# Kernel optimization log

Measured on AMD Instinct MI355X. Metric: run time of the kernel, lower is better.

The kernel has to match this reference:

```python
import jax, jax.numpy as jnp
import numpy as np
from jax import lax

B, L, V = 128, 64, 8192
E = H = 128
STEPS = 10
MAX_BIN = 512
BETA_START, BETA_END = 1e-4, 2e-2


def setup_inputs():
    key = jax.random.key(0)
    k = jax.random.split(key, 23)
    s = 0.05
    padded_x = (jax.random.uniform(k[0], (B, L, V)) < 0.01).astype(jnp.float32)
    lengths = jax.random.randint(k[1], (B,), 1, L + 1)
    visit_mask = (jnp.arange(L)[None, :] < lengths[:, None]).astype(jnp.float32)
    padded_bins = jnp.sort(jax.random.randint(k[2], (B, L), 0, MAX_BIN), axis=1)
    t_diff = jax.random.randint(k[3], (B,), 1, STEPS + 1)
    eps = jax.random.normal(k[4], (B, L, E))
    z0 = jax.random.normal(k[5], (B, L, E))
    noise = jax.random.normal(k[6], (STEPS, B, L, E))
    W_visit = jax.random.normal(k[7], (E, V)) * s
    bin_embed = (jax.random.normal(k[8], (MAX_BIN + 2, E)) * s).at[0].set(0.0)  # padding_idx=0
    W_ih = jax.random.normal(k[9], (4 * H, E)) * s
    W_hh = jax.random.normal(k[10], (4 * H, H)) * s
    b_ih = jax.random.normal(k[11], (4 * H,)) * s
    b_hh = jax.random.normal(k[12], (4 * H,)) * s
    W_cls = jax.random.normal(k[13], (1, H)) * s
    b_cls = jax.random.normal(k[14], (1,)) * s
    W_proj = jax.random.normal(k[15], (E, H)) * s
    time_embed = jax.random.normal(k[16], (STEPS + 1, E)) * s
    W_fuse = jax.random.normal(k[17], (2, 2 * E)) * s
    b_fuse = jax.random.normal(k[18], (2,)) * s
    W_e1 = jax.random.normal(k[19], (E, 2 * E)) * s
    b_e1 = jax.random.normal(k[20], (E,)) * s
    W_e2 = jax.random.normal(k[21], (E, E)) * s
    b_e2 = jax.random.normal(k[22], (E,)) * s
    return dict(padded_x=padded_x, visit_mask=visit_mask, padded_bins=padded_bins,
                t_diff=t_diff, eps=eps, z0=z0, noise=noise, W_visit=W_visit,
                bin_embed=bin_embed, W_ih=W_ih, W_hh=W_hh, b_ih=b_ih, b_hh=b_hh,
                W_cls=W_cls, b_cls=b_cls, W_proj=W_proj, time_embed=time_embed,
                W_fuse=W_fuse, b_fuse=b_fuse, W_e1=W_e1, b_e1=b_e1, W_e2=W_e2, b_e2=b_e2)


def _lstm(v, W_ih, W_hh, b_ih, b_hh):
    # v: [B,L,E] -> h: [B,L,H]; PyTorch gate order i,f,g,o
    xg = jnp.einsum('ble,ge->blg', v, W_ih) + b_ih + b_hh
    def step(carry, x):
        h, c = carry
        g = x + h @ W_hh.T
        i, f, gg, o = jnp.split(g, 4, axis=-1)
        c = jax.nn.sigmoid(f) * c + jax.nn.sigmoid(i) * jnp.tanh(gg)
        h = jax.nn.sigmoid(o) * jnp.tanh(c)
        return (h, c), h
    z = jnp.zeros((v.shape[0], W_hh.shape[1]), v.dtype)
    _, hs = lax.scan(step, (z, z), jnp.swapaxes(xg, 0, 1))
    return jnp.swapaxes(hs, 0, 1)


def _last_hidden(h, mask):
    lengths = jnp.maximum(mask.sum(axis=1).astype(jnp.int32), 1)
    return h[jnp.arange(h.shape[0]), lengths - 1]


def reference(padded_x, visit_mask, padded_bins, t_diff, eps, z0, noise,
              W_visit, bin_embed, W_ih, W_hh, b_ih, b_hh, W_cls, b_cls,
              W_proj, time_embed, W_fuse, b_fuse, W_e1, b_e1, W_e2, b_e2):
    m = visit_mask[..., None]                      # [B,L,1]
    betas = jnp.linspace(BETA_START, BETA_END, STEPS)
    alphas = 1.0 - betas
    alpha_bars = jnp.cumprod(alphas)

    # visit embedding + time-gap (delta bin) embedding
    delta = jnp.concatenate([jnp.zeros_like(padded_bins[:, :1]),
                             jnp.clip(padded_bins[:, 1:] - padded_bins[:, :-1], 0)], axis=1)
    delta = jnp.where(visit_mask > 0, jnp.clip(delta, 0, MAX_BIN + 1), 0)
    v = (padded_x @ W_visit.T + bin_embed[delta]) * m  # [B,L,E]

    # encoder LSTM (packed seq == plain scan then zero padded suffix positions)
    h = _lstm(v, W_ih, W_hh, b_ih, b_hh) * m
    logits_real = (_last_hidden(h, visit_mask) @ W_cls.T + b_cls)[:, 0]

    h_prev = jnp.pad(h[:, :-1], ((0, 0), (1, 0), (0, 0)))
    hp = (h_prev @ W_proj.T) * m                   # [B,L,E]

    def fuse_eps(z, t_emb):
        a = jax.nn.softmax(jnp.concatenate([z, hp], -1) @ W_fuse.T + b_fuse, axis=-1)
        g = a[..., :1] * z + a[..., 1:] * hp
        x = jnp.concatenate([g, t_emb], -1)
        return jax.nn.relu(x @ W_e1.T + b_e1) @ W_e2.T + b_e2

    # diffusion loss
    t = jnp.where(visit_mask > 0, t_diff[:, None], 1)    # [B,L]
    ab = alpha_bars[t - 1][..., None]
    z_t = (jnp.sqrt(ab) * v + jnp.sqrt(1.0 - ab) * eps) * m
    eps_pred = fuse_eps(z_t, time_embed[t])
    denom = jnp.maximum(visit_mask.sum(), 1.0)
    diffusion_loss = jnp.sum((eps_pred - eps) ** 2 * m) / denom

    # reverse diffusion sampling of synthetic visit embeddings
    def step(z, inp):
        kk, nz = inp
        t_s = jnp.where(visit_mask > 0, kk, 1)
        e = fuse_eps(z, time_embed[t_s])
        beta = betas[kk - 1]
        mean = (z - beta / jnp.sqrt(1.0 - alpha_bars[kk - 1]) * e) / jnp.sqrt(alphas[kk - 1])
        z = jnp.where(kk > 1, mean + jnp.sqrt(beta) * nz, mean) * m
        return z, None

    ks = jnp.arange(STEPS, 0, -1)
    v_syn, _ = lax.scan(step, z0, (ks, noise))

    h_syn = _lstm(v_syn, W_ih, W_hh, b_ih, b_hh) * m
    logits_syn = (_last_hidden(h_syn, visit_mask) @ W_cls.T + b_cls)[:, 0]
    return logits_real, logits_syn, diffusion_loss
```

## Files before the change

### kernel.cpp

```cpp
#include <hip/hip_runtime.h>

#define B_ 128
#define L_ 64
#define V_ 8192
#define E_ 128
#define H_ 128
#define G4_ 512
#define NROW (B_*L_)
#define HSTRIDE 136
#define AS 136
#define XS 264
#define YS 136
#define ZS 132

typedef unsigned short u16;
typedef __attribute__((ext_vector_type(8))) short bf16x8;
typedef __attribute__((ext_vector_type(4))) float f32x4;

__device__ __forceinline__ float sigm(float x){ return 1.f/(1.f + __expf(-x)); }
__device__ __forceinline__ float ftanh(float x){ float e = __expf(2.f*x); return 1.f - 2.f/(e + 1.f); }
__device__ __forceinline__ u16 f2bf(float f){
    union { unsigned int i; float f; } x; x.f = f;
    unsigned int r = x.i + 0x7fff + ((x.i >> 16) & 1);
    return (u16)(r >> 16);
}
#define LBAR() asm volatile("s_waitcnt lgkmcnt(0)\ns_barrier" ::: "memory")

__device__ __forceinline__ bf16x8 pack8(const float* p){
    const float4* q = (const float4*)p;
    float4 a = q[0], b = q[1];
    bf16x8 f;
    f[0]=(short)f2bf(a.x); f[1]=(short)f2bf(a.y); f[2]=(short)f2bf(a.z); f[3]=(short)f2bf(a.w);
    f[4]=(short)f2bf(b.x); f[5]=(short)f2bf(b.y); f[6]=(short)f2bf(b.z); f[7]=(short)f2bf(b.w);
    return f;
}

__global__ __launch_bounds__(256) void k_transpose_wv(const float* __restrict__ Wv, float* __restrict__ WT){
    __shared__ float tile[16][129];
    int v0 = blockIdx.x * 16;
    int t = threadIdx.x;
    #pragma unroll
    for(int i=0;i<8;i++){
        int idx = i*256 + t; int e = idx >> 4; int vv = idx & 15;
        tile[vv][e] = Wv[(size_t)e*V_ + v0 + vv];
    }
    __syncthreads();
    #pragma unroll
    for(int i=0;i<8;i++){
        int idx = i*256 + t; int vv = idx >> 7; int e = idx & 127;
        WT[(size_t)(v0+vv)*E_ + e] = tile[vv][e];
    }
}

__global__ __launch_bounds__(256) void k_visit_embed(const float* __restrict__ px, const float* __restrict__ vmask,
                                                     const int* __restrict__ bins, const float* __restrict__ bemb,
                                                     const float* __restrict__ WT, float* __restrict__ v){
    __shared__ int idxs[512];
    __shared__ int cnt;
    __shared__ int dsh;
    __shared__ float msh;
    int row = blockIdx.x; int l = row & 63;
    int t = threadIdx.x;
    if(t==0){
        cnt = 0;
        float m = vmask[row];
        int d = 0;
        if(l > 0){ d = bins[row] - bins[row-1]; d = d < 0 ? 0 : (d > 513 ? 513 : d); }
        if(!(m > 0.f)) d = 0;
        dsh = d; msh = m;
    }
    __syncthreads();
    const uint4* xr4 = (const uint4*)(px + (size_t)row * V_);
    for(int i=t;i<2048;i+=256){
        uint4 u = xr4[i];
        unsigned int w[4] = {u.x,u.y,u.z,u.w};
        #pragma unroll
        for(int j=0;j<4;j++){
            if(w[j]){ int p = atomicAdd(&cnt,1); if(p<512) idxs[p] = i*4 + j; }
        }
    }
    __syncthreads();
    int n = cnt; if(n > 512) n = 512;
    float m = msh;
    if(t < 128){
        float acc = bemb[dsh*E_ + t];
        for(int j=0;j<n;j++) acc += WT[(size_t)idxs[j]*E_ + t];
        v[(size_t)row*E_ + t] = acc * m;
    }
}

__global__ __launch_bounds__(256,2) void k_gemm_xg(const float* __restrict__ A, const float* __restrict__ Wih,
                                                   const float* __restrict__ bih, const float* __restrict__ bhh,
                                                   float* __restrict__ xg){
    __shared__ __align__(16) u16 abuf[16*AS];
    int t = threadIdx.x, wave = t >> 6, lane = t & 63, quad = lane >> 4, lc = lane & 15;
    int row0 = blockIdx.x * 16;
    #pragma unroll
    for(int i=0;i<8;i++){
        int flat = i*256 + t; int r = flat >> 7, e = flat & 127;
        abuf[r*AS + e] = f2bf(A[(size_t)(row0+r)*E_ + e]);
    }
    bf16x8 wfr[8][4]; float bb[8];
    #pragma unroll
    for(int nt=0;nt<8;nt++){
        int n = wave*128 + nt*16 + lc;
        bb[nt] = bih[n] + bhh[n];
        const float* wr = Wih + (size_t)n*E_ + quad*8;
        #pragma unroll
        for(int kt=0;kt<4;kt++) wfr[nt][kt] = pack8(wr + kt*32);
    }
    __syncthreads();
    f32x4 acc[8];
    #pragma unroll
    for(int nt=0;nt<8;nt++) acc[nt] = (f32x4){0.f,0.f,0.f,0.f};
    #pragma unroll
    for(int kt=0;kt<4;kt++){
        bf16x8 af = *(const bf16x8*)&abuf[lc*AS + kt*32 + quad*8];
        #pragma unroll
        for(int nt=0;nt<8;nt++)
            acc[nt] = __builtin_amdgcn_mfma_f32_16x16x32_bf16(af, wfr[nt][kt], acc[nt], 0,0,0);
    }
    #pragma unroll
    for(int nt=0;nt<8;nt++){
        int n = wave*128 + nt*16 + lc;
        #pragma unroll
        for(int r=0;r<4;r++)
            xg[(size_t)(row0 + quad*4 + r)*G4_ + n] = acc[nt][r] + bb[nt];
    }
}

__device__ __forceinline__ void lstm_step(int l, const float* pxg, float* ph,
        const u16* bufr, u16* bufw, const bf16x8 (&bf)[4][2][4],
        float (&xcur)[4][2][4], float (&xnxt)[4][2][4], float (&c8)[2][4],
        const float* vmsh, int lc, int quad, int wave, bool pf){
    bf16x8 af[4];
    #pragma unroll
    for(int kt=0;kt<4;kt++)
        af[kt] = *(const bf16x8*)&bufr[lc*HSTRIDE + kt*32 + quad*8];
    if(pf){
        #pragma unroll
        for(int gate=0;gate<4;gate++){
            #pragma unroll
            for(int ji=0;ji<2;ji++){
                #pragma unroll
                for(int r=0;r<4;r++)
                    xnxt[gate][ji][r] = pxg[(size_t)r*64*G4_ + (size_t)(l+1)*G4_ + gate*128 + ji*16];
            }
        }
    }
    f32x4 acc[8];
    #pragma unroll
    for(int a=0;a<8;a++) acc[a] = (f32x4){0.f,0.f,0.f,0.f};
    #pragma unroll
    for(int kt=0;kt<4;kt++){
        #pragma unroll
        for(int a=0;a<8;a++)
            acc[a] = __builtin_amdgcn_mfma_f32_16x16x32_bf16(af[kt], bf[a>>1][a&1][kt], acc[a], 0,0,0);
    }
    #pragma unroll
    for(int r=0;r<4;r++){
        float m = vmsh[(quad*4+r)*64 + l];
        #pragma unroll
        for(int ji=0;ji<2;ji++){
            float gi = acc[0+ji][r] + xcur[0][ji][r];
            float gf = acc[2+ji][r] + xcur[1][ji][r];
            float gg = acc[4+ji][r] + xcur[2][ji][r];
            float go = acc[6+ji][r] + xcur[3][ji][r];
            float c  = sigm(gf)*c8[ji][r] + sigm(gi)*ftanh(gg);
            float h  = sigm(go)*ftanh(c);
            c8[ji][r] = c;
            bufw[(quad*4+r)*HSTRIDE + wave*32 + ji*16 + lc] = f2bf(h);
            ph[(size_t)r*64*H_ + (size_t)l*H_ + ji*16] = h * m;
        }
    }
    LBAR();
}

__global__ __launch_bounds__(256,1) void k_lstm_mfma(const float* __restrict__ xg, const float* __restrict__ Whh,
                                                     const float* __restrict__ vmask, float* __restrict__ hout){
    __shared__ u16 hbuf[2][16*HSTRIDE];
    __shared__ float vmsh[16*64];
    int t = threadIdx.x;
    int wave = t >> 6, lane = t & 63;
    int quad = lane >> 4, lc = lane & 15;
    int b0 = blockIdx.x * 16;

    for(int i=t;i<16*HSTRIDE;i+=256) hbuf[0][i] = 0;
    for(int i=t;i<1024;i+=256) vmsh[i] = vmask[b0*64 + i];

    bf16x8 bf[4][2][4];
    #pragma unroll
    for(int gate=0;gate<4;gate++){
        #pragma unroll
        for(int ji=0;ji<2;ji++){
            int n = gate*128 + wave*32 + ji*16 + lc;
            const float* wr = Whh + (size_t)n*H_ + quad*8;
            #pragma unroll
            for(int kt=0;kt<4;kt++) bf[gate][ji][kt] = pack8(wr + kt*32);
        }
    }

    float c8[2][4];
    #pragma unroll
    for(int ji=0;ji<2;ji++){
        #pragma unroll
        for(int r=0;r<4;r++) c8[ji][r]=0.f;
    }

    const float* pxg = xg + ((size_t)(b0 + quad*4))*64*G4_ + wave*32 + lc;
    float* ph = hout + ((size_t)(b0 + quad*4))*64*H_ + wave*32 + lc;

    float xgv0[4][2][4], xgv1[4][2][4];
    #pragma unroll
    for(int gate=0;gate<4;gate++){
        #pragma unroll
        for(int ji=0;ji<2;ji++){
            #pragma unroll
            for(int r=0;r<4;r++)
                xgv0[gate][ji][r] = pxg[(size_t)r*64*G4_ + gate*128 + ji*16];
        }
    }
    __syncthreads();

    for(int lb=0;lb<64;lb+=2){
        lstm_step(lb,   pxg, ph, hbuf[0], hbuf[1], bf, xgv0, xgv1, c8, vmsh, lc, quad, wave, true);
        lstm_step(lb+1, pxg, ph, hbuf[1], hbuf[0], bf, xgv1, xgv0, c8, vmsh, lc, quad, wave, (lb+1) < 63);
    }
}

__global__ __launch_bounds__(256,2) void k_hp(const float* __restrict__ h, const float* __restrict__ Wproj,
                                              const float* __restrict__ vmask, float* __restrict__ hp){
    __shared__ __align__(16) u16 abuf[16*AS];
    int t = threadIdx.x, wave = t >> 6, lane = t & 63, quad = lane >> 4, lc = lane & 15;
    int row0 = blockIdx.x * 16;
    #pragma unroll
    for(int i=0;i<8;i++){
        int flat = i*256 + t; int r = flat >> 7, e = flat & 127;
        int row = row0 + r;
        float hv = (row & 63) ? h[(size_t)(row-1)*H_ + e] : 0.f;
        abuf[r*AS + e] = f2bf(hv);
    }
    bf16x8 wfr[2][4];
    #pragma unroll
    for(int nt=0;nt<2;nt++){
        int n = wave*32 + nt*16 + lc;
        const float* wr = Wproj + (size_t)n*H_ + quad*8;
        #pragma unroll
        for(int kt=0;kt<4;kt++) wfr[nt][kt] = pack8(wr + kt*32);
    }
    __syncthreads();
    f32x4 acc[2];
    acc[0] = (f32x4){0.f,0.f,0.f,0.f}; acc[1] = (f32x4){0.f,0.f,0.f,0.f};
    #pragma unroll
    for(int kt=0;kt<4;kt++){
        bf16x8 af = *(const bf16x8*)&abuf[lc*AS + kt*32 + quad*8];
        acc[0] = __builtin_amdgcn_mfma_f32_16x16x32_bf16(af, wfr[0][kt], acc[0], 0,0,0);
        acc[1] = __builtin_amdgcn_mfma_f32_16x16x32_bf16(af, wfr[1][kt], acc[1], 0,0,0);
    }
    #pragma unroll
    for(int nt=0;nt<2;nt++){
        int n = wave*32 + nt*16 + lc;
        #pragma unroll
        for(int r=0;r<4;r++){
            int row = row0 + quad*4 + r;
            hp[(size_t)row*E_ + n] = acc[nt][r] * vmask[row];
        }
    }
}

__global__ void k_logits(const float* __restrict__ h, const float* __restrict__ vmask,
                         const float* __restrict__ Wcls, const float* __restrict__ bcls, float* __restrict__ out){
    int b = blockIdx.x; int t = threadIdx.x;
    float s = vmask[b*64 + t];
    #pragma unroll
    for(int off=32;off;off>>=1) s += __shfl_down(s, off);
    s = __shfl(s, 0);
    int len = (int)(s + 0.5f); if(len < 1) len = 1;
    const float* hr = h + (size_t)(b*64 + len - 1)*H_;
    float val = hr[t]*Wcls[t] + hr[t+64]*Wcls[t+64];
    #pragma unroll
    for(int off=32;off;off>>=1) val += __shfl_down(val, off);
    if(t==0) out[b] = val + bcls[0];
}

__global__ __launch_bounds__(256,1) void k_diff_loss_mfma(const float* __restrict__ v, const float* __restrict__ hp,
        const float* __restrict__ eps, const int* __restrict__ tdiff, const float* __restrict__ vmask,
        const float* __restrict__ temb, const float* __restrict__ Wf, const float* __restrict__ bfu,
        const float* __restrict__ We1, const float* __restrict__ be1,
        const float* __restrict__ We2, const float* __restrict__ be2, float* __restrict__ lossacc){
    __shared__ float zbuf[16*ZS], hpbuf[16*ZS];
    __shared__ __align__(16) u16 xbuf[16*XS];
    __shared__ __align__(16) u16 y1buf[16*YS];
    __shared__ float wfsh[512];
    __shared__ float ssh[16][2], hpd[16][2];
    __shared__ float mrow[16]; __shared__ int trow[16];
    __shared__ float sabar[10];
    int row0 = blockIdx.x * 16; int t = threadIdx.x;
    int wave = t >> 6, lane = t & 63, quad = lane >> 4, lc = lane & 15;

    if(t==0){
        float p = 1.f;
        for(int k=0;k<10;k++){ float b = 1e-4f + (0.02f - 1e-4f)*k/9.f; p *= (1.f - b); sabar[k] = p; }
    }
    if(t < 16){
        int row = row0 + t; float m = vmask[row];
        mrow[t] = m; trow[t] = (m > 0.f) ? tdiff[row >> 6] : 1;
    }
    for(int i=t;i<512;i+=256) wfsh[i] = Wf[i];
    __syncthreads();
    #pragma unroll
    for(int i=0;i<8;i++){
        int flat = i*256 + t; int r = flat >> 7; int e = flat & 127; int row = row0 + r;
        float ab = sabar[trow[r]-1];
        zbuf[r*ZS + e] = (sqrtf(ab)*v[(size_t)row*E_ + e] + sqrtf(1.f - ab)*eps[(size_t)row*E_ + e]) * mrow[r];
        hpbuf[r*ZS + e] = hp[(size_t)row*E_ + e];
    }
    bf16x8 wf1[2][8], wf2[2][4];
    float be1v[2], be2v[2];
    #pragma unroll
    for(int nt=0;nt<2;nt++){
        int n = wave*32 + nt*16 + lc;
        be1v[nt] = be1[n]; be2v[nt] = be2[n];
        const float* w1 = We1 + (size_t)n*256 + quad*8;
        #pragma unroll
        for(int kt=0;kt<8;kt++) wf1[nt][kt] = pack8(w1 + kt*32);
        const float* w2 = We2 + (size_t)n*128 + quad*8;
        #pragma unroll
        for(int kt=0;kt<4;kt++) wf2[nt][kt] = pack8(w2 + kt*32);
    }
    __syncthreads();
    {
        int row = t >> 4, k = (t >> 3) & 1, sub = t & 7;
        float p = 0.f, q = 0.f;
        #pragma unroll
        for(int i=0;i<16;i++){
            p += hpbuf[row*ZS + sub*16 + i] * wfsh[k*256 + 128 + sub*16 + i];
            q += zbuf[row*ZS + sub*16 + i]  * wfsh[k*256 + sub*16 + i];
        }
        p += __shfl_down(p,4); p += __shfl_down(p,2); p += __shfl_down(p,1);
        q += __shfl_down(q,4); q += __shfl_down(q,2); q += __shfl_down(q,1);
        if(sub == 0){ hpd[row][k] = p + bfu[k]; ssh[row][k] = q; }
    }
    __syncthreads();
    {
        int row = t >> 4, c0 = (t & 15) * 16;
        float s0 = ssh[row][0] + hpd[row][0], s1 = ssh[row][1] + hpd[row][1];
        float a0 = 1.f/(1.f + __expf(s1 - s0)), a1 = 1.f - a0;
        int tt = trow[row];
        #pragma unroll
        for(int i=0;i<16;i++){
            int c = c0 + i;
            float val = (c < 128) ? (a0*zbuf[row*ZS + c] + a1*hpbuf[row*ZS + c])
                                  : temb[tt*E_ + (c - 128)];
            xbuf[row*XS + c] = f2bf(val);
        }
    }
    __syncthreads();
    f32x4 acc1[2];
    acc1[0] = (f32x4){0.f,0.f,0.f,0.f}; acc1[1] = (f32x4){0.f,0.f,0.f,0.f};
    #pragma unroll
    for(int kt=0;kt<8;kt++){
        bf16x8 af = *(const bf16x8*)&xbuf[lc*XS + kt*32 + quad*8];
        acc1[0] = __builtin_amdgcn_mfma_f32_16x16x32_bf16(af, wf1[0][kt], acc1[0], 0,0,0);
        acc1[1] = __builtin_amdgcn_mfma_f32_16x16x32_bf16(af, wf1[1][kt], acc1[1], 0,0,0);
    }
    #pragma unroll
    for(int nt=0;nt<2;nt++){
        #pragma unroll
        for(int r=0;r<4;r++)
            y1buf[(quad*4+r)*YS + wave*32 + nt*16 + lc] = f2bf(fmaxf(acc1[nt][r] + be1v[nt], 0.f));
    }
    __syncthreads();
    f32x4 acc2[2];
    acc2[0] = (f32x4){0.f,0.f,0.f,0.f}; acc2[1] = (f32x4){0.f,0.f,0.f,0.f};
    #pragma unroll
    for(int kt=0;kt<4;kt++){
        bf16x8 af = *(const bf16x8*)&y1buf[lc*YS + kt*32 + quad*8];
        acc2[0] = __builtin_amdgcn_mfma_f32_16x16x32_bf16(af, wf2[0][kt], acc2[0], 0,0,0);
        acc2[1] = __builtin_amdgcn_mfma_f32_16x16x32_bf16(af, wf2[1][kt], acc2[1], 0,0,0);
    }
    float lp = 0.f;
    #pragma unroll
    for(int nt=0;nt<2;nt++){
        int n = wave*32 + nt*16 + lc;
        #pragma unroll
        for(int r=0;r<4;r++){
            int m = quad*4 + r;
            float d = (acc2[nt][r] + be2v[nt]) - eps[(size_t)(row0+m)*E_ + n];
            lp += d*d*mrow[m];
        }
    }
    #pragma unroll
    for(int off=32;off;off>>=1) lp += __shfl_down(lp, off);
    if(lane == 0) atomicAdd(lossacc, lp);
}

__global__ __launch_bounds__(256,1) void k_reverse_mfma(const float* __restrict__ hp, const float* __restrict__ z0,
        const float* __restrict__ noise, const float* __restrict__ vmask, const float* __restrict__ temb,
        const float* __restrict__ Wf, const float* __restrict__ bfu,
        const float* __restrict__ We1, const float* __restrict__ be1,
        const float* __restrict__ We2, const float* __restrict__ be2, float* __restrict__ vsyn){
    __shared__ float zbuf[16*ZS], hpbuf[16*ZS];
    __shared__ __align__(16) u16 xbuf[16*XS];
    __shared__ __align__(16) u16 y1buf[16*YS];
    __shared__ float wfsh[512];
    __shared__ float ssh[16][2], hpd[16][2];
    __shared__ float mrow[16];
    __shared__ float sbeta[10], sabar[10];
    int row0 = blockIdx.x * 16; int t = threadIdx.x;
    int wave = t >> 6, lane = t & 63, quad = lane >> 4, lc = lane & 15;

    if(t==0){
        float p = 1.f;
        for(int k=0;k<10;k++){ float b = 1e-4f + (0.02f - 1e-4f)*k/9.f; sbeta[k] = b; p *= (1.f - b); sabar[k] = p; }
    }
    if(t < 16) mrow[t] = vmask[row0 + t];
    for(int i=t;i<512;i+=256) wfsh[i] = Wf[i];
    #pragma unroll
    for(int i=0;i<8;i++){
        int flat = i*256 + t; int r = flat >> 7; int e = flat & 127; int row = row0 + r;
        zbuf[r*ZS + e]  = z0[(size_t)row*E_ + e];
        hpbuf[r*ZS + e] = hp[(size_t)row*E_ + e];
    }
    bf16x8 wf1[2][8], wf2[2][4];
    float be1v[2], be2v[2];
    #pragma unroll
    for(int nt=0;nt<2;nt++){
        int n = wave*32 + nt*16 + lc;
        be1v[nt] = be1[n]; be2v[nt] = be2[n];
        const float* w1 = We1 + (size_t)n*256 + quad*8;
        #pragma unroll
        for(int kt=0;kt<8;kt++) wf1[nt][kt] = pack8(w1 + kt*32);
        const float* w2 = We2 + (size_t)n*128 + quad*8;
        #pragma unroll
        for(int kt=0;kt<4;kt++) wf2[nt][kt] = pack8(w2 + kt*32);
    }
    __syncthreads();
    {
        int row = t >> 4, k = (t >> 3) & 1, sub = t & 7;
        float p = 0.f;
        #pragma unroll
        for(int i=0;i<16;i++)
            p += hpbuf[row*ZS + sub*16 + i] * wfsh[k*256 + 128 + sub*16 + i];
        p += __shfl_down(p,4); p += __shfl_down(p,2); p += __shfl_down(p,1);
        if(sub == 0) hpd[row][k] = p + bfu[k];
    }
    __syncthreads();

    for(int s=0;s<10;s++){
        int kk = 10 - s;
        {
            int row = t >> 4, k = (t >> 3) & 1, sub = t & 7;
            float q = 0.f;
            #pragma unroll
            for(int i=0;i<16;i++)
                q += zbuf[row*ZS + sub*16 + i] * wfsh[k*256 + sub*16 + i];
            q += __shfl_down(q,4); q += __shfl_down(q,2); q += __shfl_down(q,1);
            if(sub == 0) ssh[row][k] = q + hpd[row][k];
        }
        __syncthreads();
        {
            int row = t >> 4, c0 = (t & 15) * 16;
            float s0 = ssh[row][0], s1 = ssh[row][1];
            float a0 = 1.f/(1.f + __expf(s1 - s0)), a1 = 1.f - a0;
            int tt = (mrow[row] > 0.f) ? kk : 1;
            #pragma unroll
            for(int i=0;i<16;i++){
                int c = c0 + i;
                float val = (c < 128) ? (a0*zbuf[row*ZS + c] + a1*hpbuf[row*ZS + c])
                                      : temb[tt*E_ + (c - 128)];
                xbuf[row*XS + c] = f2bf(val);
            }
        }
        __syncthreads();
        f32x4 acc1[2];
        acc1[0] = (f32x4){0.f,0.f,0.f,0.f}; acc1[1] = (f32x4){0.f,0.f,0.f,0.f};
        #pragma unroll
        for(int kt=0;kt<8;kt++){
            bf16x8 af = *(const bf16x8*)&xbuf[lc*XS + kt*32 + quad*8];
            acc1[0] = __builtin_amdgcn_mfma_f32_16x16x32_bf16(af, wf1[0][kt], acc1[0], 0,0,0);
            acc1[1] = __builtin_amdgcn_mfma_f32_16x16x32_bf16(af, wf1[1][kt], acc1[1], 0,0,0);
        }
        #pragma unroll
        for(int nt=0;nt<2;nt++){
            #pragma unroll
            for(int r=0;r<4;r++)
                y1buf[(quad*4+r)*YS + wave*32 + nt*16 + lc] = f2bf(fmaxf(acc1[nt][r] + be1v[nt], 0.f));
        }
        __syncthreads();
        f32x4 acc2[2];
        acc2[0] = (f32x4){0.f,0.f,0.f,0.f}; acc2[1] = (f32x4){0.f,0.f,0.f,0.f};
        #pragma unroll
        for(int kt=0;kt<4;kt++){
            bf16x8 af = *(const bf16x8*)&y1buf[lc*YS + kt*32 + quad*8];
            acc2[0] = __builtin_amdgcn_mfma_f32_16x16x32_bf16(af, wf2[0][kt], acc2[0], 0,0,0);
            acc2[1] = __builtin_amdgcn_mfma_f32_16x16x32_bf16(af, wf2[1][kt], acc2[1], 0,0,0);
        }
        float beta = sbeta[kk-1];
        float c1 = beta / sqrtf(1.f - sabar[kk-1]);
        float c2 = 1.f / sqrtf(1.f - beta);
        float sb = sqrtf(beta);
        #pragma unroll
        for(int nt=0;nt<2;nt++){
            int n = wave*32 + nt*16 + lc;
            #pragma unroll
            for(int r=0;r<4;r++){
                int m = quad*4 + r;
                float e = acc2[nt][r] + be2v[nt];
                float z = zbuf[m*ZS + n];
                float mean = (z - c1*e) * c2;
                float nz = noise[((size_t)s*NROW + row0 + m)*E_ + n];
                float znew = (kk > 1) ? (mean + sb*nz) : mean;
                zbuf[m*ZS + n] = znew * mrow[m];
            }
        }
        __syncthreads();
    }
    {
        int row = t >> 4, c0 = (t & 15) * 16;
        if(c0 < 128){
            #pragma unroll
            for(int i=0;i<16;i++)
                vsyn[(size_t)(row0+row)*E_ + c0 + i] = zbuf[row*ZS + c0 + i];
        }
    }
}

__global__ void k_finalize(const float* __restrict__ lossacc, const float* __restrict__ vmask, float* __restrict__ out){
    __shared__ float rb[4];
    int t = threadIdx.x;
    float s = 0.f;
    for(int i=t;i<NROW;i+=256) s += vmask[i];
    #pragma unroll
    for(int off=32;off;off>>=1) s += __shfl_down(s, off);
    if((t & 63) == 0) rb[t >> 6] = s;
    __syncthreads();
    if(t == 0){
        float denom = rb[0]+rb[1]+rb[2]+rb[3];
        if(denom < 1.f) denom = 1.f;
        out[256] = lossacc[0] / denom;
    }
}

extern "C" void kernel_launch(void* const* d_in, const int* in_sizes, int n_in,
                              void* d_out, int out_size, void* d_ws, size_t ws_size,
                              hipStream_t stream){
    const float* px    = (const float*)d_in[0];
    const float* vmask = (const float*)d_in[1];
    const int*   bins  = (const int*)d_in[2];
    const int*   tdiff = (const int*)d_in[3];
    const float* eps   = (const float*)d_in[4];
    const float* z0    = (const float*)d_in[5];
    const float* noise = (const float*)d_in[6];
    const float* Wv    = (const float*)d_in[7];
    const float* bemb  = (const float*)d_in[8];
    const float* Wih   = (const float*)d_in[9];
    const float* Whh   = (const float*)d_in[10];
    const float* bih   = (const float*)d_in[11];
    const float* bhh   = (const float*)d_in[12];
    const float* Wcls  = (const float*)d_in[13];
    const float* bcls  = (const float*)d_in[14];
    const float* Wproj = (const float*)d_in[15];
    const float* temb  = (const float*)d_in[16];
    const float* Wf    = (const float*)d_in[17];
    const float* bfu   = (const float*)d_in[18];
    const float* We1   = (const float*)d_in[19];
    const float* be1   = (const float*)d_in[20];
    const float* We2   = (const float*)d_in[21];
    const float* be2   = (const float*)d_in[22];
    float* out = (float*)d_out;

    float* ws      = (float*)d_ws;
    float* WT      = ws;
    float* v       = ws + 1048576;
    float* xg      = ws + 2097152;
    float* h       = ws + 6291456;
    float* hp      = ws + 7340032;
    float* vsyn    = ws + 8388608;
    float* lossacc = ws + 9437184;

    hipLaunchKernelGGL(k_transpose_wv, dim3(V_/16), dim3(256), 0, stream, Wv, WT);
    hipLaunchKernelGGL(k_visit_embed, dim3(NROW), dim3(256), 0, stream, px, vmask, bins, bemb, WT, v);
    hipLaunchKernelGGL(k_gemm_xg, dim3(NROW/16), dim3(256), 0, stream, v, Wih, bih, bhh, xg);
    hipLaunchKernelGGL(k_lstm_mfma, dim3(B_/16), dim3(256), 0, stream, xg, Whh, vmask, h);
    hipLaunchKernelGGL(k_logits, dim3(B_), dim3(64), 0, stream, h, vmask, Wcls, bcls, out);
    hipLaunchKernelGGL(k_hp, dim3(NROW/16), dim3(256), 0, stream, h, Wproj, vmask, hp);
    hipMemsetAsync(lossacc, 0, sizeof(float), stream);
    hipLaunchKernelGGL(k_diff_loss_mfma, dim3(NROW/16), dim3(256), 0, stream,
                       v, hp, eps, tdiff, vmask, temb, Wf, bfu, We1, be1, We2, be2, lossacc);
    hipLaunchKernelGGL(k_reverse_mfma, dim3(NROW/16), dim3(256), 0, stream,
                       hp, z0, noise, vmask, temb, Wf, bfu, We1, be1, We2, be2, vsyn);
    hipLaunchKernelGGL(k_gemm_xg, dim3(NROW/16), dim3(256), 0, stream, vsyn, Wih, bih, bhh, xg);
    hipLaunchKernelGGL(k_lstm_mfma, dim3(B_/16), dim3(256), 0, stream, xg, Whh, vmask, h);
    hipLaunchKernelGGL(k_logits, dim3(B_), dim3(64), 0, stream, h, vmask, Wcls, bcls, out + 128);
    hipLaunchKernelGGL(k_finalize, dim3(1), dim3(256), 0, stream, lossacc, vmask, out);
}
```

Baseline: 901.7 us.

## Parallelize visit-embed gather, widen LSTM to 8 waves, drop loss atomics

The visit-embedding gather now uses all 256 threads, each loading float4 rows across 8 index groups, followed by a shared-memory reduction. Before, only 128 threads did scalar loads. The LSTM recurrence kernel uses 512 threads (8 waves), each handling 16 hidden units instead of 32, so each sequential step has less per-wave MFMA and activation work. The diffusion-loss atomic is replaced by per-block partial sums that the finalize kernel reduces, which also removes the memset. Launch bounds on the two diffusion kernels are raised to 2 blocks per CU, which may add register pressure.

Result: faster. 828.7 us (-8.1%).

```diff
diff --git a/kernel.cpp b/kernel.cpp
--- a/kernel.cpp
+++ b/kernel.cpp
@@ -59,6 +59,7 @@
     __shared__ int cnt;
     __shared__ int dsh;
     __shared__ float msh;
+    __shared__ float4 red[8][32];
     int row = blockIdx.x; int l = row & 63;
     int t = threadIdx.x;
     if(t==0){
@@ -81,11 +82,28 @@
     }
     __syncthreads();
     int n = cnt; if(n > 512) n = 512;
-    float m = msh;
-    if(t < 128){
-        float acc = bemb[dsh*E_ + t];
-        for(int j=0;j<n;j++) acc += WT[(size_t)idxs[j]*E_ + t];
-        v[(size_t)row*E_ + t] = acc * m;
+    int eq = t & 31, jg = t >> 5;
+    float4 a4 = {0.f,0.f,0.f,0.f};
+    for(int j=jg;j<n;j+=8){
+        const float4* wr = (const float4*)(WT + (size_t)idxs[j]*E_);
+        float4 wv = wr[eq];
+        a4.x += wv.x; a4.y += wv.y; a4.z += wv.z; a4.w += wv.w;
+    }
+    red[jg][eq] = a4;
+    __syncthreads();
+    if(t < 32){
+        float4 s = red[0][t];
+        #pragma unroll
+        for(int g=1;g<8;g++){
+            float4 r = red[g][t];
+            s.x += r.x; s.y += r.y; s.z += r.z; s.w += r.w;
+        }
+        const float4* bp = (const float4*)(bemb + dsh*E_);
+        float4 bv = bp[t];
+        float m = msh;
+        float4 o;
+        o.x = (s.x + bv.x)*m; o.y = (s.y + bv.y)*m; o.z = (s.z + bv.z)*m; o.w = (s.w + bv.w)*m;
+        ((float4*)(v + (size_t)row*E_))[t] = o;
     }
 }
 
@@ -130,8 +148,8 @@
 }
 
 __device__ __forceinline__ void lstm_step(int l, const float* pxg, float* ph,
-        const u16* bufr, u16* bufw, const bf16x8 (&bf)[4][2][4],
-        float (&xcur)[4][2][4], float (&xnxt)[4][2][4], float (&c8)[2][4],
+        const u16* bufr, u16* bufw, const bf16x8 (&bf)[4][4],
+        float (&xcur)[4][4], float (&xnxt)[4][4], float (&c4)[4],
         const float* vmsh, int lc, int quad, int wave, bool pf){
     bf16x8 af[4];
     #pragma unroll
@@ -141,42 +159,36 @@
         #pragma unroll
         for(int gate=0;gate<4;gate++){
             #pragma unroll
-            for(int ji=0;ji<2;ji++){
-                #pragma unroll
-                for(int r=0;r<4;r++)
-                    xnxt[gate][ji][r] = pxg[(size_t)r*64*G4_ + (size_t)(l+1)*G4_ + gate*128 + ji*16];
-            }
-        }
-    }
-    f32x4 acc[8];
-    #pragma unroll
-    for(int a=0;a<8;a++) acc[a] = (f32x4){0.f,0.f,0.f,0.f};
+            for(int r=0;r<4;r++)
+                xnxt[gate][r] = pxg[(size_t)r*64*G4_ + (size_t)(l+1)*G4_ + gate*128];
+        }
+    }
+    f32x4 acc[4];
+    #pragma unroll
+    for(int a=0;a<4;a++) acc[a] = (f32x4){0.f,0.f,0.f,0.f};
     #pragma unroll
     for(int kt=0;kt<4;kt++){
         #pragma unroll
-        for(int a=0;a<8;a++)
-            acc[a] = __builtin_amdgcn_mfma_f32_16x16x32_bf16(af[kt], bf[a>>1][a&1][kt], acc[a], 0,0,0);
+        for(int a=0;a<4;a++)
+            acc[a] = __builtin_amdgcn_mfma_f32_16x16x32_bf16(af[kt], bf[a][kt], acc[a], 0,0,0);
     }
     #pragma unroll
     for(int r=0;r<4;r++){
         float m = vmsh[(quad*4+r)*64 + l];
-        #pragma unroll
-        for(int ji=0;ji<2;ji++){
-            float gi = acc[0+ji][r] + xcur[0][ji][r];
-            float gf = acc[2+ji][r] + xcur[1][ji][r];
-            float gg = acc[4+ji][r] + xcur[2][ji][r];
-            float go = acc[6+ji][r] + xcur[3][ji][r];
-            float c  = sigm(gf)*c8[ji][r] + sigm(gi)*ftanh(gg);
-            float h  = sigm(go)*ftanh(c);
-            c8[ji][r] = c;
-            bufw[(quad*4+r)*HSTRIDE + wave*32 + ji*16 + lc] = f2bf(h);
-            ph[(size_t)r*64*H_ + (size_t)l*H_ + ji*16] = h * m;
-        }
+        float gi = acc[0][r] + xcur[0][r];
+        float gf = acc[1][r] + xcur[1][r];
+        float gg = acc[2][r] + xcur[2][r];
+        float go = acc[3][r] + xcur[3][r];
+        float c  = sigm(gf)*c4[r] + sigm(gi)*ftanh(gg);
+        float h  = sigm(go)*ftanh(c);
+        c4[r] = c;
+        bufw[(quad*4+r)*HSTRIDE + wave*16 + lc] = f2bf(h);
+        ph[(size_t)r*64*H_ + (size_t)l*H_] = h * m;
     }
     LBAR();
 }
 
-__global__ __launch_bounds__(256,1) void k_lstm_mfma(const float* __restrict__ xg, const float* __restrict__ Whh,
+__global__ __launch_bounds__(512,2) void k_lstm_mfma(const float* __restrict__ xg, const float* __restrict__ Whh,
                                                      const float* __restrict__ vmask, float* __restrict__ hout){
     __shared__ u16 hbuf[2][16*HSTRIDE];
     __shared__ float vmsh[16*64];
@@ -185,46 +197,35 @@
     int quad = lane >> 4, lc = lane & 15;
     int b0 = blockIdx.x * 16;
 
-    for(int i=t;i<16*HSTRIDE;i+=256) hbuf[0][i] = 0;
-    for(int i=t;i<1024;i+=256) vmsh[i] = vmask[b0*64 + i];
-
-    bf16x8 bf[4][2][4];
+    for(int i=t;i<16*HSTRIDE;i+=512) hbuf[0][i] = 0;
+    for(int i=t;i<1024;i+=512) vmsh[i] = vmask[b0*64 + i];
+
+    bf16x8 bf[4][4];
     #pragma unroll
     for(int gate=0;gate<4;gate++){
-        #pragma unroll
-        for(int ji=0;ji<2;ji++){
-            int n = gate*128 + wave*32 + ji*16 + lc;
-            const float* wr = Whh + (size_t)n*H_ + quad*8;
-            #pragma unroll
-            for(int kt=0;kt<4;kt++) bf[gate][ji][kt] = pack8(wr + kt*32);
-        }
-    }
-
-    float c8[2][4];
-    #pragma unroll
-    for(int ji=0;ji<2;ji++){
-        #pragma unroll
-        for(int r=0;r<4;r++) c8[ji][r]=0.f;
-    }
-
-    const float* pxg = xg + ((size_t)(b0 + quad*4))*64*G4_ + wave*32 + lc;
-    float* ph = hout + ((size_t)(b0 + quad*4))*64*H_ + wave*32 + lc;
-
-    float xgv0[4][2][4], xgv1[4][2][4];
+        int n = gate*128 + wave*16 + lc;
+        const float* wr = Whh + (size_t)n*H_ + quad*8;
+        #pragma unroll
+        for(int kt=0;kt<4;kt++) bf[gate][kt] = pack8(wr + kt*32);
+    }
+
+    float c4[4] = {0.f,0.f,0.f,0.f};
+
+    const float* pxg = xg + ((size_t)(b0 + quad*4))*64*G4_ + wave*16 + lc;
+    float* ph = hout + ((size_t)(b0 + quad*4))*64*H_ + wave*16 + lc;
+
+    float xgv0[4][4], xgv1[4][4];
     #pragma unroll
     for(int gate=0;gate<4;gate++){
         #pragma unroll
-        for(int ji=0;ji<2;ji++){
-            #pragma unroll
-            for(int r=0;r<4;r++)
-                xgv0[gate][ji][r] = pxg[(size_t)r*64*G4_ + gate*128 + ji*16];
-        }
+        for(int r=0;r<4;r++)
+            xgv0[gate][r] = pxg[(size_t)r*64*G4_ + gate*128];
     }
     __syncthreads();
 
     for(int lb=0;lb<64;lb+=2){
-        lstm_step(lb,   pxg, ph, hbuf[0], hbuf[1], bf, xgv0, xgv1, c8, vmsh, lc, quad, wave, true);
-        lstm_step(lb+1, pxg, ph, hbuf[1], hbuf[0], bf, xgv1, xgv0, c8, vmsh, lc, quad, wave, (lb+1) < 63);
+        lstm_step(lb,   pxg, ph, hbuf[0], hbuf[1], bf, xgv0, xgv1, c4, vmsh, lc, quad, wave, true);
+        lstm_step(lb+1, pxg, ph, hbuf[1], hbuf[0], bf, xgv1, xgv0, c4, vmsh, lc, quad, wave, (lb+1) < 63);
     }
 }
 
@@ -283,11 +284,11 @@
     if(t==0) out[b] = val + bcls[0];
 }
 
-__global__ __launch_bounds__(256,1) void k_diff_loss_mfma(const float* __restrict__ v, const float* __restrict__ hp,
+__global__ __launch_bounds__(256,2) void k_diff_loss_mfma(const float* __restrict__ v, const float* __restrict__ hp,
         const float* __restrict__ eps, const int* __restrict__ tdiff, const float* __restrict__ vmask,
         const float* __restrict__ temb, const float* __restrict__ Wf, const float* __restrict__ bfu,
         const float* __restrict__ We1, const float* __restrict__ be1,
-        const float* __restrict__ We2, const float* __restrict__ be2, float* __restrict__ lossacc){
+        const float* __restrict__ We2, const float* __restrict__ be2, float* __restrict__ partial){
     __shared__ float zbuf[16*ZS], hpbuf[16*ZS];
     __shared__ __align__(16) u16 xbuf[16*XS];
     __shared__ __align__(16) u16 y1buf[16*YS];
@@ -295,6 +296,7 @@
     __shared__ float ssh[16][2], hpd[16][2];
     __shared__ float mrow[16]; __shared__ int trow[16];
     __shared__ float sabar[10];
+    __shared__ float rb[4];
     int row0 = blockIdx.x * 16; int t = threadIdx.x;
     int wave = t >> 6, lane = t & 63, quad = lane >> 4, lc = lane & 15;
 
@@ -392,10 +394,12 @@
     }
     #pragma unroll
     for(int off=32;off;off>>=1) lp += __shfl_down(lp, off);
-    if(lane == 0) atomicAdd(lossacc, lp);
-}
-
-__global__ __launch_bounds__(256,1) void k_reverse_mfma(const float* __restrict__ hp, const float* __restrict__ z0,
+    if(lane == 0) rb[wave] = lp;
+    __syncthreads();
+    if(t == 0) partial[blockIdx.x] = rb[0]+rb[1]+rb[2]+rb[3];
+}
+
+__global__ __launch_bounds__(256,2) void k_reverse_mfma(const float* __restrict__ hp, const float* __restrict__ z0,
         const float* __restrict__ noise, const float* __restrict__ vmask, const float* __restrict__ temb,
         const float* __restrict__ Wf, const float* __restrict__ bfu,
         const float* __restrict__ We1, const float* __restrict__ be1,
@@ -526,19 +530,21 @@
     }
 }
 
-__global__ void k_finalize(const float* __restrict__ lossacc, const float* __restrict__ vmask, float* __restrict__ out){
-    __shared__ float rb[4];
+__global__ void k_finalize(const float* __restrict__ partial, const float* __restrict__ vmask, float* __restrict__ out){
+    __shared__ float rb[4], rl[4];
     int t = threadIdx.x;
     float s = 0.f;
     for(int i=t;i<NROW;i+=256) s += vmask[i];
-    #pragma unroll
-    for(int off=32;off;off>>=1) s += __shfl_down(s, off);
-    if((t & 63) == 0) rb[t >> 6] = s;
+    float ls = 0.f;
+    for(int i=t;i<512;i+=256) ls += partial[i];
+    #pragma unroll
+    for(int off=32;off;off>>=1){ s += __shfl_down(s, off); ls += __shfl_down(ls, off); }
+    if((t & 63) == 0){ rb[t >> 6] = s; rl[t >> 6] = ls; }
     __syncthreads();
     if(t == 0){
         float denom = rb[0]+rb[1]+rb[2]+rb[3];
         if(denom < 1.f) denom = 1.f;
-        out[256] = lossacc[0] / denom;
+        out[256] = (rl[0]+rl[1]+rl[2]+rl[3]) / denom;
     }
 }
 
@@ -577,21 +583,20 @@
     float* h       = ws + 6291456;
     float* hp      = ws + 7340032;
     float* vsyn    = ws + 8388608;
-    float* lossacc = ws + 9437184;
+    float* partial = ws + 9437184;
 
     hipLaunchKernelGGL(k_transpose_wv, dim3(V_/16), dim3(256), 0, stream, Wv, WT);
     hipLaunchKernelGGL(k_visit_embed, dim3(NROW), dim3(256), 0, stream, px, vmask, bins, bemb, WT, v);
     hipLaunchKernelGGL(k_gemm_xg, dim3(NROW/16), dim3(256), 0, stream, v, Wih, bih, bhh, xg);
-    hipLaunchKernelGGL(k_lstm_mfma, dim3(B_/16), dim3(256), 0, stream, xg, Whh, vmask, h);
+    hipLaunchKernelGGL(k_lstm_mfma, dim3(B_/16), dim3(512), 0, stream, xg, Whh, vmask, h);
     hipLaunchKernelGGL(k_logits, dim3(B_), dim3(64), 0, stream, h, vmask, Wcls, bcls, out);
     hipLaunchKernelGGL(k_hp, dim3(NROW/16), dim3(256), 0, stream, h, Wproj, vmask, hp);
-    hipMemsetAsync(lossacc, 0, sizeof(float), stream);
     hipLaunchKernelGGL(k_diff_loss_mfma, dim3(NROW/16), dim3(256), 0, stream,
-                       v, hp, eps, tdiff, vmask, temb, Wf, bfu, We1, be1, We2, be2, lossacc);
+                       v, hp, eps, tdiff, vmask, temb, Wf, bfu, We1, be1, We2, be2, partial);
     hipLaunchKernelGGL(k_reverse_mfma, dim3(NROW/16), dim3(256), 0, stream,
                        hp, z0, noise, vmask, temb, Wf, bfu, We1, be1, We2, be2, vsyn);
     hipLaunchKernelGGL(k_gemm_xg, dim3(NROW/16), dim3(256), 0, stream, vsyn, Wih, bih, bhh, xg);
-    hipLaunchKernelGGL(k_lstm_mfma, dim3(B_/16), dim3(256), 0, stream, xg, Whh, vmask, h);
+    hipLaunchKernelGGL(k_lstm_mfma, dim3(B_/16), dim3(512), 0, stream, xg, Whh, vmask, h);
     hipLaunchKernelGGL(k_logits, dim3(B_), dim3(64), 0, stream, h, vmask, Wcls, bcls, out + 128);
-    hipLaunchKernelGGL(k_finalize, dim3(1), dim3(256), 0, stream, lossacc, vmask, out);
-}
+    hipLaunchKernelGGL(k_finalize, dim3(1), dim3(256), 0, stream, partial, vmask, out);
+}
```
